# Performance work log

Hardware: AMD Instinct MI355X
Metric: run time of the kernel (lower is better)

## Reference

```python
import jax, jax.numpy as jnp
import numpy as np

B, N, C = 2, 4096, 256
H = 8          # num heads
D = C // H     # head dim = 32
SR = 2         # spatial reduction ratio
HID = 1024     # mixffn hidden = 4*C
EPS = 1e-5


def layernorm(x, g, b):
    mu = jnp.mean(x, axis=-1, keepdims=True)
    var = jnp.mean(jnp.square(x - mu), axis=-1, keepdims=True)
    return (x - mu) * jax.lax.rsqrt(var + EPS) * g + b


def conv2d(x, w, b, stride, pad, groups=1):
    out = jax.lax.conv_general_dilated(
        x, w, (stride, stride), [(pad, pad), (pad, pad)],
        dimension_numbers=("NCHW", "OIHW", "NCHW"), feature_group_count=groups)
    return out + b[None, :, None, None]


def setup_inputs() -> dict:
    key = jax.random.key(0)
    ks = jax.random.split(key, 20)
    s = lambda k, shape, scale=0.02: jax.random.normal(k, shape, jnp.float32) * scale
    return {
        "x": jax.random.normal(ks[0], (B, N, C), jnp.float32),
        "h": 64, "w": 64,
        "ln1_g": jnp.ones((C,), jnp.float32), "ln1_b": jnp.zeros((C,), jnp.float32),
        "q_w": s(ks[1], (C, C)),
        "kv_w": s(ks[2], (2 * C, C)),
        "sr_w": s(ks[3], (C, C, SR, SR)), "sr_b": jnp.zeros((C,), jnp.float32),
        "srn_g": jnp.ones((C,), jnp.float32), "srn_b": jnp.zeros((C,), jnp.float32),
        "proj_w": s(ks[4], (C, C)), "proj_b": jnp.zeros((C,), jnp.float32),
        "ln2_g": jnp.ones((C,), jnp.float32), "ln2_b": jnp.zeros((C,), jnp.float32),
        "fc1_w": s(ks[5], (HID, C)), "fc1_b": jnp.zeros((HID,), jnp.float32),
        "pe_w": s(ks[6], (HID, 1, 3, 3)), "pe_b": jnp.zeros((HID,), jnp.float32),
        "fc2_w": s(ks[7], (C, HID)), "fc2_b": jnp.zeros((C,), jnp.float32),
    }


def reference(x, h, w, ln1_g, ln1_b, q_w, kv_w, sr_w, sr_b, srn_g, srn_b,
              proj_w, proj_b, ln2_g, ln2_b, fc1_w, fc1_b, pe_w, pe_b, fc2_w, fc2_b):
    b_, n_, c_ = x.shape
    # ---- attention branch ----
    xn = layernorm(x, ln1_g, ln1_b)
    q = jnp.einsum("bnc,oc->bno", xn, q_w).reshape(b_, n_, H, D).transpose(0, 2, 1, 3)  # [B,H,N,D]
    # spatial-reduction of KV
    x_kv = xn.reshape(b_, h, w, c_).transpose(0, 3, 1, 2)              # [B,C,h,w]
    x_kv = conv2d(x_kv, sr_w, sr_b, stride=SR, pad=0)                  # [B,C,h/SR,w/SR]
    nkv = (h // SR) * (w // SR)
    x_kv = x_kv.reshape(b_, c_, nkv).transpose(0, 2, 1)                # [B,Nkv,C]
    x_kv = layernorm(x_kv, srn_g, srn_b)
    kv = jnp.einsum("bnc,oc->bno", x_kv, kv_w).reshape(b_, nkv, 2, H, D)
    k = kv[:, :, 0].transpose(0, 2, 1, 3)                              # [B,H,Nkv,D]
    v = kv[:, :, 1].transpose(0, 2, 1, 3)
    scale = D ** -0.5
    att = jax.nn.softmax(jnp.einsum("bhxd,bhyd->bhxy", q, k) * scale, axis=-1)
    o = jnp.einsum("bhxy,bhyd->bhxd", att, v)                          # [B,H,N,D]
    o = o.transpose(0, 2, 1, 3).reshape(b_, n_, c_)
    o = jnp.einsum("bnc,oc->bno", o, proj_w) + proj_b
    x = x + o
    # ---- Mix-FFN branch ----
    xn2 = layernorm(x, ln2_g, ln2_b)
    xf = xn2.reshape(b_, h, w, c_).transpose(0, 3, 1, 2)               # [B,C,h,w]
    xf = jnp.einsum("bchw,oc->bohw", xf, fc1_w) + fc1_b[None, :, None, None]
    xf = conv2d(xf, pe_w, pe_b, stride=1, pad=1, groups=HID)           # depthwise 3x3
    xf = jax.nn.gelu(xf, approximate=False)
    xf = jnp.einsum("bchw,oc->bohw", xf, fc2_w) + fc2_b[None, :, None, None]
    xf = xf.transpose(0, 2, 3, 1).reshape(b_, n_, c_)
    return x + xf
```

## Files before the change

kernel.cpp:

```cpp
#include <hip/hip_runtime.h>
#include <math.h>

constexpr int BB   = 2;
constexpr int NN   = 4096;
constexpr int CCH  = 256;
constexpr int NH   = 8;
constexpr int HD   = 32;
constexpr int GW   = 64;
constexpr int NKV  = 1024;
constexpr int HIDN = 1024;
constexpr float EPSF = 1e-5f;

typedef short  bf16x8 __attribute__((ext_vector_type(8)));
typedef short  bf16x4 __attribute__((ext_vector_type(4)));
typedef float  f32x4  __attribute__((ext_vector_type(4)));

__device__ __forceinline__ short f2bf(float f) {
    unsigned int u = __float_as_uint(f);
    unsigned int r = (u + 0x7FFFu + ((u >> 16) & 1u)) >> 16;
    return (short)r;
}
__device__ __forceinline__ float bf2f(short s) {
    return __uint_as_float(((unsigned int)(unsigned short)s) << 16);
}
__device__ __forceinline__ void gl16(const void* g, void* l) {
    __builtin_amdgcn_global_load_lds(
        (const __attribute__((address_space(1))) void*)g,
        (__attribute__((address_space(3))) void*)l, 16, 0, 0);
}

__global__ __launch_bounds__(256) void prep_kernel(const float* __restrict__ q_w,
                                                   const float* __restrict__ kv_w,
                                                   const float* __restrict__ proj_w,
                                                   const float* __restrict__ fc1_w,
                                                   const float* __restrict__ fc2_w,
                                                   const float* __restrict__ sr_w,
                                                   short* qwb, short* kvwb, short* pjwb,
                                                   short* f1wb, short* f2wb, short* srwb,
                                                   const float* __restrict__ x,
                                                   const float* __restrict__ ln1_g,
                                                   const float* __restrict__ ln1_b,
                                                   short* __restrict__ xn) {
    __shared__ float pa[4], pb[4];
    int t = threadIdx.x;
    if (blockIdx.x < 4096) {
        int i = blockIdx.x * 256 + t;
        if (i < 65536) { qwb[i] = f2bf(q_w[i] * 0.17677669529663687f); return; }
        i -= 65536;
        if (i < 131072) { kvwb[i] = f2bf(kv_w[i]); return; }
        i -= 131072;
        if (i < 65536) { pjwb[i] = f2bf(proj_w[i]); return; }
        i -= 65536;
        if (i < 262144) { f1wb[i] = f2bf(fc1_w[i]); return; }
        i -= 262144;
        if (i < 262144) { f2wb[i] = f2bf(fc2_w[i]); return; }
        i -= 262144;
        srwb[i] = f2bf(sr_w[i]);
        return;
    }
    int row = blockIdx.x - 4096;
    float v = x[row * CCH + t];
    float a = v, b = v * v;
#pragma unroll
    for (int off = 32; off > 0; off >>= 1) {
        a += __shfl_xor(a, off);
        b += __shfl_xor(b, off);
    }
    int w = t >> 6;
    if ((t & 63) == 0) { pa[w] = a; pb[w] = b; }
    __syncthreads();
    a = pa[0] + pa[1] + pa[2] + pa[3];
    b = pb[0] + pb[1] + pb[2] + pb[3];
    float mu = a * (1.0f / CCH);
    float var = b * (1.0f / CCH) - mu * mu;
    float rs = rsqrtf(var + EPSF);
    xn[row * CCH + t] = f2bf((v - mu) * rs * ln1_g[t] + ln1_b[t]);
}

template <bool INBF>
__global__ __launch_bounds__(256) void ln_kernel(const void* __restrict__ in,
                                                 const float* __restrict__ g,
                                                 const float* __restrict__ bta,
                                                 short* __restrict__ out) {
    int row = blockIdx.x;
    int t = threadIdx.x;
    float v = INBF ? bf2f(((const short*)in)[row * CCH + t])
                   : ((const float*)in)[row * CCH + t];
    float a = v, b = v * v;
#pragma unroll
    for (int off = 32; off > 0; off >>= 1) {
        a += __shfl_xor(a, off);
        b += __shfl_xor(b, off);
    }
    __shared__ float pa[4], pb[4];
    int w = t >> 6;
    if ((t & 63) == 0) { pa[w] = a; pb[w] = b; }
    __syncthreads();
    a = pa[0] + pa[1] + pa[2] + pa[3];
    b = pb[0] + pb[1] + pb[2] + pb[3];
    float mu = a * (1.0f / CCH);
    float var = b * (1.0f / CCH) - mu * mu;
    float rs = rsqrtf(var + EPSF);
    out[row * CCH + t] = f2bf((v - mu) * rs * g[t] + bta[t]);
}

template <bool OUTB, int RESMODE>
__global__ __launch_bounds__(256, 4) void gemm64(const short* __restrict__ A,
                                                 const short* __restrict__ W,
                                                 const float* __restrict__ bias,
                                                 const void* __restrict__ res,
                                                 void* __restrict__ outp,
                                                 int M, int O, int K) {
    __shared__ short As0[64][64], Ws0[64][64];
    __shared__ short As1[64][64], Ws1[64][64];
    int t = threadIdx.x;
    int m0 = blockIdx.y * 64, o0 = blockIdx.x * 64;
    int w = t >> 6, lane = t & 63;
    int wm = (w >> 1) * 32, wn = (w & 1) * 32;
    int fr = lane & 15, fq = lane >> 4;
    int srow = lane >> 3;
    int sg   = (lane & 7) ^ srow;
    f32x4 acc[2][2];
#pragma unroll
    for (int mi = 0; mi < 2; mi++)
#pragma unroll
        for (int ni = 0; ni < 2; ni++)
            acc[mi][ni] = f32x4{0.f, 0.f, 0.f, 0.f};

    auto stage = [&](short (*Asb)[64], short (*Wsb)[64], int k0) {
#pragma unroll
        for (int r = 0; r < 2; r++) {
            int rowA = r * 32 + w * 8 + srow;
            gl16(&A[(size_t)(m0 + rowA) * K + k0 + sg * 8], &Asb[r * 32 + w * 8][0]);
            gl16(&W[(size_t)(o0 + rowA) * K + k0 + sg * 8], &Wsb[r * 32 + w * 8][0]);
        }
    };
    auto compute = [&](short (*Asb)[64], short (*Wsb)[64]) {
#pragma unroll
        for (int half = 0; half < 2; half++) {
            bf16x8 af[2], wf[2];
#pragma unroll
            for (int mi = 0; mi < 2; mi++) {
                int row = wm + mi * 16 + fr;
                af[mi] = *(const bf16x8*)&Asb[row][(((half << 2) | fq) ^ (row & 7)) * 8];
            }
#pragma unroll
            for (int ni = 0; ni < 2; ni++) {
                int row = wn + ni * 16 + fr;
                wf[ni] = *(const bf16x8*)&Wsb[row][(((half << 2) | fq) ^ (row & 7)) * 8];
            }
#pragma unroll
            for (int mi = 0; mi < 2; mi++)
#pragma unroll
                for (int ni = 0; ni < 2; ni++)
                    acc[mi][ni] = __builtin_amdgcn_mfma_f32_16x16x32_bf16(
                        af[mi], wf[ni], acc[mi][ni], 0, 0, 0);
        }
    };

    stage(As0, Ws0, 0);
    __syncthreads();
    for (int k0 = 0; k0 < K; k0 += 128) {
        if (k0 + 64 < K) stage(As1, Ws1, k0 + 64);
        compute(As0, Ws0);
        __syncthreads();
        if (k0 + 128 < K) stage(As0, Ws0, k0 + 128);
        if (k0 + 64 < K) compute(As1, Ws1);
        __syncthreads();
    }
#pragma unroll
    for (int mi = 0; mi < 2; mi++)
#pragma unroll
        for (int ni = 0; ni < 2; ni++)
#pragma unroll
            for (int r = 0; r < 4; r++) {
                int m = m0 + wm + mi * 16 + fq * 4 + r;
                int o = o0 + wn + ni * 16 + fr;
                float v = acc[mi][ni][r];
                if (bias) v += bias[o];
                if (RESMODE == 1) v += ((const float*)res)[(size_t)m * O + o];
                if (RESMODE == 2) v += bf2f(((const short*)res)[(size_t)m * O + o]);
                if (OUTB) ((short*)outp)[(size_t)m * O + o] = f2bf(v);
                else      ((float*)outp)[(size_t)m * O + o] = v;
            }
}

__global__ __launch_bounds__(256) void im2col_sr(const short* __restrict__ xn,
                                                 short* __restrict__ kvin) {
    int blk = blockIdx.x;
    int b = blk >> 10, p = blk & 1023;
    int i = p >> 5, j = p & 31;
    int t = threadIdx.x;
    bf16x4 v;
#pragma unroll
    for (int q = 0; q < 4; q++) {
        int di = q >> 1, dj = q & 1;
        v[q] = xn[((size_t)(b * NN) + (2 * i + di) * GW + 2 * j + dj) * CCH + t];
    }
    *(bf16x4*)&kvin[(size_t)blk * 1024 + t * 4] = v;
}

__global__ __launch_bounds__(256, 4) void kv_gemm(const short* __restrict__ A,
                                                  const short* __restrict__ W,
                                                  short* __restrict__ kvk,
                                                  short* __restrict__ vt) {
    __shared__ short As0[64][64], Ws0[64][64];
    __shared__ short As1[64][64], Ws1[64][64];
    int t = threadIdx.x;
    int m0 = blockIdx.y * 64, o0 = blockIdx.x * 64;
    int w = t >> 6, lane = t & 63;
    int wm = (w >> 1) * 32, wn = (w & 1) * 32;
    int fr = lane & 15, fq = lane >> 4;
    int srow = lane >> 3;
    int sg   = (lane & 7) ^ srow;
    f32x4 acc[2][2];
#pragma unroll
    for (int mi = 0; mi < 2; mi++)
#pragma unroll
        for (int ni = 0; ni < 2; ni++)
            acc[mi][ni] = f32x4{0.f, 0.f, 0.f, 0.f};

    auto stage = [&](short (*Asb)[64], short (*Wsb)[64], int k0) {
#pragma unroll
        for (int r = 0; r < 2; r++) {
            int rowA = r * 32 + w * 8 + srow;
            gl16(&A[(size_t)(m0 + rowA) * CCH + k0 + sg * 8], &Asb[r * 32 + w * 8][0]);
            gl16(&W[(size_t)(o0 + rowA) * CCH + k0 + sg * 8], &Wsb[r * 32 + w * 8][0]);
        }
    };
    auto compute = [&](short (*Asb)[64], short (*Wsb)[64]) {
#pragma unroll
        for (int half = 0; half < 2; half++) {
            bf16x8 af[2], wf[2];
#pragma unroll
            for (int mi = 0; mi < 2; mi++) {
                int row = wm + mi * 16 + fr;
                af[mi] = *(const bf16x8*)&Asb[row][(((half << 2) | fq) ^ (row & 7)) * 8];
            }
#pragma unroll
            for (int ni = 0; ni < 2; ni++) {
                int row = wn + ni * 16 + fr;
                wf[ni] = *(const bf16x8*)&Wsb[row][(((half << 2) | fq) ^ (row & 7)) * 8];
            }
#pragma unroll
            for (int mi = 0; mi < 2; mi++)
#pragma unroll
                for (int ni = 0; ni < 2; ni++)
                    acc[mi][ni] = __builtin_amdgcn_mfma_f32_16x16x32_bf16(
                        af[mi], wf[ni], acc[mi][ni], 0, 0, 0);
        }
    };

    stage(As0, Ws0, 0);
    __syncthreads();
    stage(As1, Ws1, 64);
    compute(As0, Ws0);
    __syncthreads();
    stage(As0, Ws0, 128);
    compute(As1, Ws1);
    __syncthreads();
    stage(As1, Ws1, 192);
    compute(As0, Ws0);
    __syncthreads();
    compute(As1, Ws1);

#pragma unroll
    for (int mi = 0; mi < 2; mi++)
#pragma unroll
        for (int ni = 0; ni < 2; ni++) {
            int o = o0 + wn + ni * 16 + fr;
            int mbase = m0 + wm + mi * 16 + fq * 4;
            if (o < 256) {
#pragma unroll
                for (int r = 0; r < 4; r++)
                    kvk[(size_t)(mbase + r) * 256 + o] = f2bf(acc[mi][ni][r]);
            } else {
                int h = (o - 256) >> 5, d = (o - 256) & 31;
                int b = mbase >> 10, y0 = mbase & 1023;
                bf16x4 pv;
#pragma unroll
                for (int r = 0; r < 4; r++) pv[r] = f2bf(acc[mi][ni][r]);
                *(bf16x4*)&vt[((size_t)((b * NH + h) * HD) + d) * NKV + y0] = pv;
            }
        }
}

__global__ __launch_bounds__(256, 4) void attn_mfma(const short* __restrict__ qb,
                                                    const short* __restrict__ kvk,
                                                    const short* __restrict__ vt,
                                                    short* __restrict__ o) {
    int blk = blockIdx.x;
    int qt = blk & 63; int hh = (blk >> 6) & 7; int b = blk >> 9;
    int t = threadIdx.x; int w = t >> 6; int lane = t & 63;
    int fr = lane & 15, fq = lane >> 4;
    __shared__ short Ks0[128][32], Ks1[128][32];
    __shared__ short Vt0[64][64],  Vt1[64][64];
    __shared__ short Ps[4][16][64];
    int n0 = qt * 64 + w * 16;
    bf16x8 qa = *(const bf16x8*)&qb[((size_t)(b * NN) + n0 + fr) * CCH + hh * HD + fq * 8];
    f32x4 oacc[2];
    float lst[4] = {0.f, 0.f, 0.f, 0.f};
#pragma unroll
    for (int nd = 0; nd < 2; nd++) oacc[nd] = f32x4{0.f, 0.f, 0.f, 0.f};

    int srowK = lane >> 2;
    int sgK   = (lane & 3) ^ (srowK & 3);
    int srowV = lane >> 3;
    int sgV   = (lane & 7) ^ srowV;

    auto stageKV = [&](short (*Ksb)[32], short (*Vtb)[64], int y0) {
#pragma unroll
        for (int r2 = 0; r2 < 2; r2++) {
            int rowK = r2 * 64 + w * 16 + srowK;
            gl16(&kvk[((size_t)(b * NKV) + y0 + rowK) * 256 + hh * HD + sgK * 8],
                 &Ksb[r2 * 64 + w * 16][0]);
        }
#pragma unroll
        for (int r3 = 0; r3 < 2; r3++) {
            int d = w * 8 + srowV;
            gl16(&vt[((size_t)((b * NH + hh) * HD) + d) * NKV + y0 + r3 * 64 + sgV * 8],
                 &Vtb[r3 * 32 + w * 8][0]);
        }
    };
    auto tile = [&](short (*Ksb)[32], short (*Vtb)[64]) {
#pragma unroll
        for (int h2 = 0; h2 < 2; h2++) {
            f32x4 s[4];
#pragma unroll
            for (int ni = 0; ni < 4; ni++) {
                int rowk = h2 * 64 + ni * 16 + fr;
                bf16x8 kb = *(const bf16x8*)&Ksb[rowk][(fq ^ (fr & 3)) * 8];
                s[ni] = __builtin_amdgcn_mfma_f32_16x16x32_bf16(
                    qa, kb, f32x4{0.f, 0.f, 0.f, 0.f}, 0, 0, 0);
            }
#pragma unroll
            for (int r = 0; r < 4; r++) {
                int row = fq * 4 + r;
                float psum = 0.f;
#pragma unroll
                for (int i = 0; i < 4; i++) {
                    float p = __expf(fminf(s[i][r], 30.f));
                    psum += p;
                    int col = i * 16 + fr;
                    int sgp = ((col >> 3) ^ row) & 7;
                    Ps[w][row][sgp * 8 + (col & 7)] = f2bf(p);
                }
                lst[r] += psum;
            }
#pragma unroll
            for (int ks = 0; ks < 2; ks++) {
                int gk = ks * 4 + fq;
                bf16x8 pa = *(const bf16x8*)&Ps[w][fr][((gk ^ fr) & 7) * 8];
#pragma unroll
                for (int nd = 0; nd < 2; nd++) {
                    int rowv = nd * 16 + fr;
                    bf16x8 vb = *(const bf16x8*)&Vtb[h2 * 32 + rowv][((gk ^ (rowv & 7)) & 7) * 8];
                    oacc[nd] = __builtin_amdgcn_mfma_f32_16x16x32_bf16(
                        pa, vb, oacc[nd], 0, 0, 0);
                }
            }
        }
    };

    stageKV(Ks0, Vt0, 0);
    __syncthreads();
    for (int y0 = 0; y0 < NKV; y0 += 256) {
        if (y0 + 128 < NKV) stageKV(Ks1, Vt1, y0 + 128);
        tile(Ks0, Vt0);
        __syncthreads();
        if (y0 + 256 < NKV) stageKV(Ks0, Vt0, y0 + 256);
        tile(Ks1, Vt1);
        __syncthreads();
    }
#pragma unroll
    for (int r = 0; r < 4; r++) {
        float ls = lst[r];
#pragma unroll
        for (int off = 1; off < 16; off <<= 1)
            ls += __shfl_xor(ls, off);
        float inv = 1.f / ls;
        int row = n0 + fq * 4 + r;
#pragma unroll
        for (int nd = 0; nd < 2; nd++)
            o[((size_t)(b * NN) + row) * CCH + hh * HD + nd * 16 + fr] =
                f2bf(oacc[nd][r] * inv);
    }
}

__global__ __launch_bounds__(256, 2) void dwconv_gelu(const short* __restrict__ xf,
                                                      const float* __restrict__ pe_w,
                                                      const float* __restrict__ pe_b,
                                                      short* __restrict__ out) {
    int blk = blockIdx.x;
    int cg = blk & 15, sp = (blk >> 4) & 15, b = blk >> 8;
    int r0 = (sp >> 2) * 16, c0 = (sp & 3) * 16;
    int ch0 = cg * 64;
    int t = threadIdx.x;
    __shared__ short tile[18][18][64];
    for (int idx = t; idx < 18 * 18 * 8; idx += 256) {
        int pix = idx >> 3, part = idx & 7;
        int row = pix / 18, col = pix - row * 18;
        int gr = r0 + row - 1, gc = c0 + col - 1;
        bf16x8 v = {0, 0, 0, 0, 0, 0, 0, 0};
        if (gr >= 0 && gr < 64 && gc >= 0 && gc < 64)
            v = *(const bf16x8*)&xf[((size_t)(b * NN) + gr * GW + gc) * HIDN + ch0 + part * 8];
        *(bf16x8*)&tile[row][col][part * 8] = v;
    }
    __syncthreads();
    int cl = t & 63, sg = t >> 6;
    int ch = ch0 + cl;
    float wv[9];
#pragma unroll
    for (int k = 0; k < 9; k++) wv[k] = pe_w[ch * 9 + k];
    float bias = pe_b[ch];
#pragma unroll
    for (int q = 0; q < 4; q++) {
        int lr = sg * 4 + q;
        float cA[3], cB[3], cC[3];
#pragma unroll
        for (int ki = 0; ki < 3; ki++) {
            cA[ki] = bf2f(tile[lr + ki][0][cl]);
            cB[ki] = bf2f(tile[lr + ki][1][cl]);
        }
        for (int cc = 0; cc < 16; cc++) {
#pragma unroll
            for (int ki = 0; ki < 3; ki++) cC[ki] = bf2f(tile[lr + ki][cc + 2][cl]);
            float acc = bias;
#pragma unroll
            for (int ki = 0; ki < 3; ki++)
                acc += cA[ki] * wv[ki * 3] + cB[ki] * wv[ki * 3 + 1] + cC[ki] * wv[ki * 3 + 2];
            float z = 0.7978845608f * (acc + 0.044715f * acc * acc * acc);
            float e = __expf(-2.f * fabsf(z));
            float th = (1.f - e) / (1.f + e);
            th = (z < 0.f) ? -th : th;
            float gg = 0.5f * acc * (1.f + th);
            out[((size_t)(b * NN) + (r0 + lr) * GW + c0 + cc) * HIDN + ch] = f2bf(gg);
#pragma unroll
            for (int ki = 0; ki < 3; ki++) { cA[ki] = cB[ki]; cB[ki] = cC[ki]; }
        }
    }
}

extern "C" void kernel_launch(void* const* d_in, const int* in_sizes, int n_in,
                              void* d_out, int out_size, void* d_ws, size_t ws_size,
                              hipStream_t stream) {
    const float* x      = (const float*)d_in[0];
    const float* ln1_g  = (const float*)d_in[3];
    const float* ln1_b  = (const float*)d_in[4];
    const float* q_w    = (const float*)d_in[5];
    const float* kv_w   = (const float*)d_in[6];
    const float* sr_w   = (const float*)d_in[7];
    const float* sr_b   = (const float*)d_in[8];
    const float* srn_g  = (const float*)d_in[9];
    const float* srn_b  = (const float*)d_in[10];
    const float* proj_w = (const float*)d_in[11];
    const float* proj_b = (const float*)d_in[12];
    const float* ln2_g  = (const float*)d_in[13];
    const float* ln2_b  = (const float*)d_in[14];
    const float* fc1_w  = (const float*)d_in[15];
    const float* fc1_b  = (const float*)d_in[16];
    const float* pe_w   = (const float*)d_in[17];
    const float* pe_b   = (const float*)d_in[18];
    const float* fc2_w  = (const float*)d_in[19];
    const float* fc2_b  = (const float*)d_in[20];
    float* out = (float*)d_out;

    char* base = (char*)d_ws;
    short* xn    = (short*)(base);
    short* qb    = (short*)(base + (4ull  << 20));
    short* kvin  = (short*)(base + (8ull  << 20));
    float* srtmp = (float*)(base + (12ull << 20));
    short* xkvn  = (short*)(base + (14ull << 20));
    short* kvk   = (short*)(base + (15ull << 20));
    short* vtb   = (short*)(base + (17ull << 20));
    short* obf   = (short*)(base + (18ull << 20));
    short* x1    = (short*)(base + (22ull << 20));
    short* xf1   = (short*)(base + (30ull << 20));
    short* xf2g  = (short*)(base + (46ull << 20));
    short* qwb   = (short*)(base + (62ull << 20));
    short* kvwb  = qwb  + 65536;
    short* pjwb  = kvwb + 131072;
    short* f1wb  = pjwb + 65536;
    short* f2wb  = f1wb + 262144;
    short* srwb  = f2wb + 262144;

    prep_kernel<<<4096 + BB * NN, 256, 0, stream>>>(q_w, kv_w, proj_w, fc1_w, fc2_w, sr_w,
                                                    qwb, kvwb, pjwb, f1wb, f2wb, srwb,
                                                    x, ln1_g, ln1_b, xn);
    {
        dim3 g(CCH / 64, (BB * NN) / 64);
        gemm64<true, 0><<<g, 256, 0, stream>>>(xn, qwb, nullptr, nullptr, qb, BB * NN, CCH, CCH);
    }
    im2col_sr<<<BB * NKV, 256, 0, stream>>>(xn, kvin);
    {
        dim3 g(CCH / 64, (BB * NKV) / 64);
        gemm64<false, 0><<<g, 256, 0, stream>>>(kvin, srwb, sr_b, nullptr, srtmp, BB * NKV, CCH, 1024);
    }
    ln_kernel<false><<<BB * NKV, 256, 0, stream>>>(srtmp, srn_g, srn_b, xkvn);
    {
        dim3 g(512 / 64, (BB * NKV) / 64);
        kv_gemm<<<g, 256, 0, stream>>>(xkvn, kvwb, kvk, vtb);
    }
    attn_mfma<<<BB * NH * (NN / 64), 256, 0, stream>>>(qb, kvk, vtb, obf);
    {
        dim3 g(CCH / 64, (BB * NN) / 64);
        gemm64<true, 1><<<g, 256, 0, stream>>>(obf, pjwb, proj_b, x, x1, BB * NN, CCH, CCH);
    }
    ln_kernel<true><<<BB * NN, 256, 0, stream>>>(x1, ln2_g, ln2_b, xn);
    {
        dim3 g(HIDN / 64, (BB * NN) / 64);
        gemm64<true, 0><<<g, 256, 0, stream>>>(xn, f1wb, fc1_b, nullptr, xf1, BB * NN, HIDN, CCH);
    }
    dwconv_gelu<<<BB * 256, 256, 0, stream>>>(xf1, pe_w, pe_b, xf2g);
    {
        dim3 g(CCH / 64, (BB * NN) / 64);
        gemm64<false, 2><<<g, 256, 0, stream>>>(xf2g, f2wb, fc2_b, x1, out, BB * NN, CCH, HIDN);
    }
}
```

Measured before the change: 132.4 us.

## Fuse im2col into SR conv GEMM, wave-per-row layernorm, larger fc1 tiles

The spatial-reduction conv now gathers its 2x2 patches straight from xn inside a new GEMM kernel. To allow this, the SR weights are reordered so that the K dimension runs patch-position-major. This drops the separate im2col kernel and its intermediate buffer. Layernorm now uses one wave per row with vector loads, removing shared-memory reductions and block syncs. fc1 uses a new 128x128-tile GEMM for more data reuse, at the cost of lower occupancy and fewer blocks.

```diff
diff --git a/kernel.cpp b/kernel.cpp
--- a/kernel.cpp
+++ b/kernel.cpp
@@ -55,7 +55,10 @@
         i -= 262144;
         if (i < 262144) { f2wb[i] = f2bf(fc2_w[i]); return; }
         i -= 262144;
-        srwb[i] = f2bf(sr_w[i]);
+        {
+            int o = i >> 10, rem = i & 1023, c = rem >> 2, q = rem & 3;
+            srwb[o * 1024 + q * 256 + c] = f2bf(sr_w[i]);
+        }
         return;
     }
     int row = blockIdx.x - 4096;
@@ -78,30 +81,37 @@
 }
 
 template <bool INBF>
-__global__ __launch_bounds__(256) void ln_kernel(const void* __restrict__ in,
-                                                 const float* __restrict__ g,
-                                                 const float* __restrict__ bta,
-                                                 short* __restrict__ out) {
-    int row = blockIdx.x;
+__global__ __launch_bounds__(256) void ln_wave(const void* __restrict__ in,
+                                               const float* __restrict__ g,
+                                               const float* __restrict__ bta,
+                                               short* __restrict__ out) {
     int t = threadIdx.x;
-    float v = INBF ? bf2f(((const short*)in)[row * CCH + t])
-                   : ((const float*)in)[row * CCH + t];
-    float a = v, b = v * v;
-#pragma unroll
-    for (int off = 32; off > 0; off >>= 1) {
+    int w = t >> 6, lane = t & 63;
+    int row = blockIdx.x * 4 + w;
+    float v[4];
+    if (INBF) {
+        bf16x4 bv = *(const bf16x4*)&((const short*)in)[(size_t)row * CCH + lane * 4];
+#pragma unroll
+        for (int j = 0; j < 4; j++) v[j] = bf2f(bv[j]);
+    } else {
+        float4 fv = *(const float4*)&((const float*)in)[(size_t)row * CCH + lane * 4];
+        v[0] = fv.x; v[1] = fv.y; v[2] = fv.z; v[3] = fv.w;
+    }
+    float a = v[0] + v[1] + v[2] + v[3];
+    float b = v[0]*v[0] + v[1]*v[1] + v[2]*v[2] + v[3]*v[3];
+#pragma unroll
+    for (int off = 1; off < 64; off <<= 1) {
         a += __shfl_xor(a, off);
         b += __shfl_xor(b, off);
     }
-    __shared__ float pa[4], pb[4];
-    int w = t >> 6;
-    if ((t & 63) == 0) { pa[w] = a; pb[w] = b; }
-    __syncthreads();
-    a = pa[0] + pa[1] + pa[2] + pa[3];
-    b = pb[0] + pb[1] + pb[2] + pb[3];
     float mu = a * (1.0f / CCH);
     float var = b * (1.0f / CCH) - mu * mu;
     float rs = rsqrtf(var + EPSF);
-    out[row * CCH + t] = f2bf((v - mu) * rs * g[t] + bta[t]);
+    bf16x4 ov;
+#pragma unroll
+    for (int j = 0; j < 4; j++)
+        ov[j] = f2bf((v[j] - mu) * rs * g[lane * 4 + j] + bta[lane * 4 + j]);
+    *(bf16x4*)&out[(size_t)row * CCH + lane * 4] = ov;
 }
 
 template <bool OUTB, int RESMODE>
@@ -185,19 +195,148 @@
             }
 }
 
-__global__ __launch_bounds__(256) void im2col_sr(const short* __restrict__ xn,
-                                                 short* __restrict__ kvin) {
-    int blk = blockIdx.x;
-    int b = blk >> 10, p = blk & 1023;
-    int i = p >> 5, j = p & 31;
+__global__ __launch_bounds__(256, 4) void sr_gemm(const short* __restrict__ xn,
+                                                  const short* __restrict__ Wsr,
+                                                  const float* __restrict__ sr_b,
+                                                  float* __restrict__ srtmp) {
+    __shared__ short As0[32][64], Ws0[64][64];
+    __shared__ short As1[32][64], Ws1[64][64];
     int t = threadIdx.x;
-    bf16x4 v;
-#pragma unroll
-    for (int q = 0; q < 4; q++) {
-        int di = q >> 1, dj = q & 1;
-        v[q] = xn[((size_t)(b * NN) + (2 * i + di) * GW + 2 * j + dj) * CCH + t];
-    }
-    *(bf16x4*)&kvin[(size_t)blk * 1024 + t * 4] = v;
+    int m0 = blockIdx.y * 32, o0 = blockIdx.x * 64;
+    int w = t >> 6, lane = t & 63;
+    int wm = (w >> 1) * 16, wn = (w & 1) * 32;
+    int fr = lane & 15, fq = lane >> 4;
+    int srow = lane >> 3;
+    int sg   = (lane & 7) ^ srow;
+    int arow = w * 8 + srow;
+    int p = m0 + arow;
+    int b = p >> 10, pp = p & 1023, ii = pp >> 5, jj = pp & 31;
+    int nbase = ii * 128 + jj * 2;
+    size_t xbase = (size_t)(b * NN) * CCH;
+    f32x4 acc[2];
+    acc[0] = f32x4{0.f, 0.f, 0.f, 0.f};
+    acc[1] = f32x4{0.f, 0.f, 0.f, 0.f};
+
+    auto stage = [&](short (*Asb)[64], short (*Wsb)[64], int k0) {
+        int q = k0 >> 8, c0 = k0 & 255;
+        int n = nbase + (q >> 1) * 64 + (q & 1);
+        gl16(&xn[xbase + (size_t)n * CCH + c0 + sg * 8], &Asb[w * 8][0]);
+#pragma unroll
+        for (int r = 0; r < 2; r++)
+            gl16(&Wsr[(size_t)(o0 + r * 32 + w * 8 + srow) * 1024 + k0 + sg * 8],
+                 &Wsb[r * 32 + w * 8][0]);
+    };
+    auto compute = [&](short (*Asb)[64], short (*Wsb)[64]) {
+#pragma unroll
+        for (int half = 0; half < 2; half++) {
+            int cg = (half << 2) | fq;
+            int rowa = wm + fr;
+            bf16x8 af = *(const bf16x8*)&Asb[rowa][(cg ^ (rowa & 7)) * 8];
+            bf16x8 wf[2];
+#pragma unroll
+            for (int ni = 0; ni < 2; ni++) {
+                int row = wn + ni * 16 + fr;
+                wf[ni] = *(const bf16x8*)&Wsb[row][(cg ^ (row & 7)) * 8];
+            }
+#pragma unroll
+            for (int ni = 0; ni < 2; ni++)
+                acc[ni] = __builtin_amdgcn_mfma_f32_16x16x32_bf16(
+                    af, wf[ni], acc[ni], 0, 0, 0);
+        }
+    };
+
+    stage(As0, Ws0, 0);
+    __syncthreads();
+    for (int k0 = 0; k0 < 1024; k0 += 128) {
+        if (k0 + 64 < 1024) stage(As1, Ws1, k0 + 64);
+        compute(As0, Ws0);
+        __syncthreads();
+        if (k0 + 128 < 1024) stage(As0, Ws0, k0 + 128);
+        compute(As1, Ws1);
+        __syncthreads();
+    }
+#pragma unroll
+    for (int ni = 0; ni < 2; ni++)
+#pragma unroll
+        for (int r = 0; r < 4; r++) {
+            int m = m0 + wm + fq * 4 + r;
+            int o = o0 + wn + ni * 16 + fr;
+            srtmp[(size_t)m * CCH + o] = acc[ni][r] + sr_b[o];
+        }
+}
+
+__global__ __launch_bounds__(256, 2) void gemm_fc1(const short* __restrict__ A,
+                                                   const short* __restrict__ W,
+                                                   const float* __restrict__ bias,
+                                                   short* __restrict__ outp,
+                                                   int M, int O, int K) {
+    __shared__ short As0[128][64], Ws0[128][64];
+    __shared__ short As1[128][64], Ws1[128][64];
+    int t = threadIdx.x;
+    int m0 = blockIdx.y * 128, o0 = blockIdx.x * 128;
+    int w = t >> 6, lane = t & 63;
+    int wm = (w >> 1) * 64, wn = (w & 1) * 64;
+    int fr = lane & 15, fq = lane >> 4;
+    int srow = lane >> 3;
+    int sg   = (lane & 7) ^ srow;
+    f32x4 acc[4][4];
+#pragma unroll
+    for (int mi = 0; mi < 4; mi++)
+#pragma unroll
+        for (int ni = 0; ni < 4; ni++)
+            acc[mi][ni] = f32x4{0.f, 0.f, 0.f, 0.f};
+
+    auto stage = [&](short (*Asb)[64], short (*Wsb)[64], int k0) {
+#pragma unroll
+        for (int r = 0; r < 4; r++) {
+            int rowA = r * 32 + w * 8 + srow;
+            gl16(&A[(size_t)(m0 + rowA) * K + k0 + sg * 8], &Asb[r * 32 + w * 8][0]);
+            gl16(&W[(size_t)(o0 + rowA) * K + k0 + sg * 8], &Wsb[r * 32 + w * 8][0]);
+        }
+    };
+    auto compute = [&](short (*Asb)[64], short (*Wsb)[64]) {
+#pragma unroll
+        for (int half = 0; half < 2; half++) {
+            bf16x8 af[4], wf[4];
+#pragma unroll
+            for (int mi = 0; mi < 4; mi++) {
+                int row = wm + mi * 16 + fr;
+                af[mi] = *(const bf16x8*)&Asb[row][(((half << 2) | fq) ^ (row & 7)) * 8];
+            }
+#pragma unroll
+            for (int ni = 0; ni < 4; ni++) {
+                int row = wn + ni * 16 + fr;
+                wf[ni] = *(const bf16x8*)&Wsb[row][(((half << 2) | fq) ^ (row & 7)) * 8];
+            }
+#pragma unroll
+            for (int mi = 0; mi < 4; mi++)
+#pragma unroll
+                for (int ni = 0; ni < 4; ni++)
+                    acc[mi][ni] = __builtin_amdgcn_mfma_f32_16x16x32_bf16(
+                        af[mi], wf[ni], acc[mi][ni], 0, 0, 0);
+        }
+    };
+
+    stage(As0, Ws0, 0);
+    __syncthreads();
+    for (int k0 = 0; k0 < K; k0 += 128) {
+        if (k0 + 64 < K) stage(As1, Ws1, k0 + 64);
+        compute(As0, Ws0);
+        __syncthreads();
+        if (k0 + 128 < K) stage(As0, Ws0, k0 + 128);
+        if (k0 + 64 < K) compute(As1, Ws1);
+        __syncthreads();
+    }
+#pragma unroll
+    for (int mi = 0; mi < 4; mi++)
+#pragma unroll
+        for (int ni = 0; ni < 4; ni++)
+#pragma unroll
+            for (int r = 0; r < 4; r++) {
+                int m = m0 + wm + mi * 16 + fq * 4 + r;
+                int o = o0 + wn + ni * 16 + fr;
+                outp[(size_t)m * O + o] = f2bf(acc[mi][ni][r] + bias[o]);
+            }
 }
 
 __global__ __launch_bounds__(256, 4) void kv_gemm(const short* __restrict__ A,
@@ -468,7 +607,6 @@
     char* base = (char*)d_ws;
     short* xn    = (short*)(base);
     short* qb    = (short*)(base + (4ull  << 20));
-    short* kvin  = (short*)(base + (8ull  << 20));
     float* srtmp = (float*)(base + (12ull << 20));
     short* xkvn  = (short*)(base + (14ull << 20));
     short* kvk   = (short*)(base + (15ull << 20));
@@ -491,12 +629,11 @@
         dim3 g(CCH / 64, (BB * NN) / 64);
         gemm64<true, 0><<<g, 256, 0, stream>>>(xn, qwb, nullptr, nullptr, qb, BB * NN, CCH, CCH);
     }
-    im2col_sr<<<BB * NKV, 256, 0, stream>>>(xn, kvin);
     {
-        dim3 g(CCH / 64, (BB * NKV) / 64);
-        gemm64<false, 0><<<g, 256, 0, stream>>>(kvin, srwb, sr_b, nullptr, srtmp, BB * NKV, CCH, 1024);
-    }
-    ln_kernel<false><<<BB * NKV, 256, 0, stream>>>(srtmp, srn_g, srn_b, xkvn);
+        dim3 g(CCH / 64, (BB * NKV) / 32);
+        sr_gemm<<<g, 256, 0, stream>>>(xn, srwb, sr_b, srtmp);
+    }
+    ln_wave<false><<<BB * NKV / 4, 256, 0, stream>>>(srtmp, srn_g, srn_b, xkvn);
     {
         dim3 g(512 / 64, (BB * NKV) / 64);
         kv_gemm<<<g, 256, 0, stream>>>(xkvn, kvwb, kvk, vtb);
@@ -506,10 +643,10 @@
         dim3 g(CCH / 64, (BB * NN) / 64);
         gemm64<true, 1><<<g, 256, 0, stream>>>(obf, pjwb, proj_b, x, x1, BB * NN, CCH, CCH);
     }
-    ln_kernel<true><<<BB * NN, 256, 0, stream>>>(x1, ln2_g, ln2_b, xn);
+    ln_wave<true><<<BB * NN / 4, 256, 0, stream>>>(x1, ln2_g, ln2_b, xn);
     {
-        dim3 g(HIDN / 64, (BB * NN) / 64);
-        gemm64<true, 0><<<g, 256, 0, stream>>>(xn, f1wb, fc1_b, nullptr, xf1, BB * NN, HIDN, CCH);
+        dim3 g(HIDN / 128, (BB * NN) / 128);
+        gemm_fc1<<<g, 256, 0, stream>>>(xn, f1wb, fc1_b, xf1, BB * NN, HIDN, CCH);
     }
     dwconv_gelu<<<BB * 256, 256, 0, stream>>>(xf1, pe_w, pe_b, xf2g);
     {
```

After: 120.0 us. -9.3%, faster.
